# Kernel tuning notes

Measured on AMD Instinct MI355X. Metric: run time of the kernel, lower is better.

Reference implementation:

```python
import jax, jax.numpy as jnp
import numpy as np

E = 128    # embedding_size
N = 8192   # total vertices (64 graphs x 128)
CN = 512   # total color slots
G = 64     # number of graphs
TMAX = 32


def _mlp3(x, W, b):
    # 3-layer MLP: Linear-ReLU-Linear-ReLU-Linear. W: [3,E,E], b: [3,E]
    h = jax.nn.relu(x @ W[0].T + b[0])
    h = jax.nn.relu(h @ W[1].T + b[1])
    return h @ W[2].T + b[2]


def _lstm_cell(x, h, c, Wih, Whh, bih, bhh):
    # PyTorch LSTM gate order: i, f, g, o
    gates = x @ Wih.T + h @ Whh.T + (bih + bhh)
    i, f, g, o = jnp.split(gates, 4, axis=-1)
    c2 = jax.nn.sigmoid(f) * c + jax.nn.sigmoid(i) * jnp.tanh(g)
    h2 = jax.nn.sigmoid(o) * jnp.tanh(c2)
    return h2, c2


def setup_inputs() -> dict:
    key = jax.random.key(0)
    ks = jax.random.split(key, 24)
    s = 1.0 / np.sqrt(E)
    f32 = jnp.float32
    inp = {
        "M_vv": jax.random.normal(ks[0], (N, N), f32) * s,
        "M_vc": jax.random.uniform(ks[1], (N, CN), f32) * (1.0 / np.sqrt(CN)),
        "C": jax.random.normal(ks[2], (CN, E), f32),
        "slice_idx": jnp.full((G,), N // G, dtype=jnp.int32),
        "v_emb_w": jax.random.normal(ks[3], (E, 1), f32) * s,
        "v_emb_b": jax.random.normal(ks[4], (E,), f32) * s,
        "mlpC_W": jax.random.normal(ks[5], (3, E, E), f32) * s,
        "mlpC_b": jax.random.normal(ks[6], (3, E), f32) * s,
        "mlpV_W": jax.random.normal(ks[7], (3, E, E), f32) * s,
        "mlpV_b": jax.random.normal(ks[8], (3, E), f32) * s,
        "Wih_v": jax.random.normal(ks[9], (4 * E, 2 * E), f32) * s,
        "Whh_v": jax.random.normal(ks[10], (4 * E, E), f32) * s,
        "bih_v": jax.random.normal(ks[11], (4 * E,), f32) * s,
        "bhh_v": jax.random.normal(ks[12], (4 * E,), f32) * s,
        "Wih_c": jax.random.normal(ks[13], (4 * E, E), f32) * s,
        "Whh_c": jax.random.normal(ks[14], (4 * E, E), f32) * s,
        "bih_c": jax.random.normal(ks[15], (4 * E,), f32) * s,
        "bhh_c": jax.random.normal(ks[16], (4 * E,), f32) * s,
        "vote_W1": jax.random.normal(ks[17], (E, E), f32) * s,
        "vote_b1": jax.random.normal(ks[18], (E,), f32) * s,
        "vote_W2": jax.random.normal(ks[19], (E, E), f32) * s,
        "vote_b2": jax.random.normal(ks[20], (E,), f32) * s,
        "vote_W3": jax.random.normal(ks[21], (1, E), f32) * s,
        "vote_b3": jax.random.normal(ks[22], (1,), f32) * s,
    }
    return inp


def reference(M_vv, M_vc, C, slice_idx, v_emb_w, v_emb_b, mlpC_W, mlpC_b,
              mlpV_W, mlpV_b, Wih_v, Whh_v, bih_v, bhh_v, Wih_c, Whh_c,
              bih_c, bhh_c, vote_W1, vote_b1, vote_W2, vote_b2, vote_W3, vote_b3):
    n = M_vv.shape[0]
    g = slice_idx.shape[0]
    # V = v_emb(ones(1)) broadcast to all vertices: [N, E]
    v0 = v_emb_w[:, 0] + v_emb_b
    V = jnp.broadcast_to(v0, (n, E))
    # Original torch loop never reassigns V, so both LSTM inputs are
    # loop-invariant; compute them once (identical math, no recompute).
    x_v = jnp.concatenate([M_vv @ V, M_vc @ _mlp3(C, mlpC_W, mlpC_b)], axis=1)  # [N, 2E]
    x_c = M_vc.T @ _mlp3(V, mlpV_W, mlpV_b)                                      # [CN, E]

    def step(carry, _):
        hv, cv, hc, cc = carry
        hv, cv = _lstm_cell(x_v, hv, cv, Wih_v, Whh_v, bih_v, bhh_v)
        hc, cc = _lstm_cell(x_c, hc, cc, Wih_c, Whh_c, bih_c, bhh_c)
        return (hv, cv, hc, cc), None

    init = (V, jnp.zeros_like(V), C, jnp.zeros_like(C))
    (hv, cv, hc, cc), _ = jax.lax.scan(step, init, None, length=TMAX)

    # vote MLP on final vertex hidden state -> [N, 1]
    h = jax.nn.relu(hv @ vote_W1.T + vote_b1)
    h = jax.nn.relu(h @ vote_W2.T + vote_b2)
    v_vote = (h @ vote_W3.T + vote_b3)[:, 0]  # [N]

    # per-graph mean then sigmoid (torch: split + mean + sigmoid + vstack)
    seg = jnp.repeat(jnp.arange(g), slice_idx, total_repeat_length=n)
    sums = jax.ops.segment_sum(v_vote, seg, num_segments=g)
    ret = jax.nn.sigmoid(sums / slice_idx.astype(sums.dtype))
    return (ret, V[None], C)
```

## Files before the change

kernel.cpp:

```cpp
#include <hip/hip_runtime.h>
#include <hip/hip_bf16.h>
#include <stdint.h>


typedef __bf16 bf16x8 __attribute__((ext_vector_type(8)));
typedef float f32x4 __attribute__((ext_vector_type(4)));

#define EDIM 128
#define NVERT 8192
#define CNUM 512
#define NG 64
#define TSTEPS 32

#define WS_CNT 0u
#define WS_V0 32768u
#define WS_W1 33280u
#define WS_BV 35328u
#define WS_ACC 37376u
#define WS_V0BF 37632u
#define WS_MLPC3T 38912u

__device__ __forceinline__ float bf2f(unsigned short s) {
  return __uint_as_float(((unsigned)s) << 16);
}
__device__ __forceinline__ unsigned short f2bf(float f) {
  unsigned u = __float_as_uint(f);
  u += 0x7fffu + ((u >> 16) & 1u);
  return (unsigned short)(u >> 16);
}
__device__ __forceinline__ float sigm(float x) {
  return __builtin_amdgcn_rcpf(1.f + __expf(-x));
}
__device__ __forceinline__ float tanh_f(float x) {
  return 1.f - 2.f * __builtin_amdgcn_rcpf(1.f + __expf(2.f * x));
}
__device__ __forceinline__ f32x4 mfma16(bf16x8 a, bf16x8 b, f32x4 c) {
  return __builtin_amdgcn_mfma_f32_16x16x32_bf16(a, b, c, 0, 0, 0);
}
__device__ __forceinline__ bf16x8 ld8(const float* p) {
  float4 a = *(const float4*)p;
  float4 b = *(const float4*)(p + 4);
  bf16x8 r;
  r[0] = (__bf16)a.x; r[1] = (__bf16)a.y; r[2] = (__bf16)a.z; r[3] = (__bf16)a.w;
  r[4] = (__bf16)b.x; r[5] = (__bf16)b.y; r[6] = (__bf16)b.z; r[7] = (__bf16)b.w;
  return r;
}

__global__ __launch_bounds__(128) void k_setup(
    const float* __restrict__ C, const float* __restrict__ W,
    const float* __restrict__ B, const float* __restrict__ vw,
    const float* __restrict__ vb, const float* __restrict__ Wih,
    const float* __restrict__ bih, const float* __restrict__ bhh,
    float* __restrict__ ws, float* __restrict__ Cout) {
  __shared__ float xb[2][EDIM];
  const int t = threadIdx.x;

  if (blockIdx.x == CNUM) {
    float* v0 = (float*)((char*)ws + WS_V0);
    float* w1 = (float*)((char*)ws + WS_W1);
    float* bvp = (float*)((char*)ws + WS_BV);
    float* acc = (float*)((char*)ws + WS_ACC);
    unsigned short* v0bf = (unsigned short*)((char*)ws + WS_V0BF);
    unsigned int* cnt = (unsigned int*)((char*)ws + WS_CNT);
    float v = vw[t] + vb[t];
    xb[0][t] = v;
    v0[t] = v;
    v0bf[t] = f2bf(v);
    if (t < NG) acc[t] = 0.f;
    if (t == 0) *cnt = 0u;
    __syncthreads();
#pragma unroll
    for (int gi = 0; gi < 4; gi++) {
      const int col = gi * EDIM + t;
      const float4* wr = (const float4*)(Wih + (size_t)col * 256);
      float s = 0.f;
#pragma unroll
      for (int kc = 0; kc < 32; kc++) {
        float4 q = wr[kc];
        const float* xi = xb[0] + kc * 4;
        s += q.x * xi[0] + q.y * xi[1] + q.z * xi[2] + q.w * xi[3];
      }
      w1[col] = s;
      bvp[col] = bih[col] + bhh[col];
    }
    return;
  }

  unsigned short* out_t = (unsigned short*)((char*)ws + WS_MLPC3T);
  const int c = blockIdx.x, e = t;
  float cval = C[c * EDIM + e];
  xb[0][e] = cval;
  Cout[c * EDIM + e] = cval;
  __syncthreads();
#pragma unroll
  for (int l = 0; l < 3; l++) {
    const float4* wrow = (const float4*)(W + ((size_t)l * EDIM + e) * EDIM);
    const float* xin = xb[l & 1];
    float s = B[l * EDIM + e];
#pragma unroll
    for (int kc = 0; kc < EDIM / 4; kc++) {
      float4 q = wrow[kc];
      const float* xi = xin + kc * 4;
      s += q.x * xi[0] + q.y * xi[1] + q.z * xi[2] + q.w * xi[3];
    }
    if (l < 2) {
      s = fmaxf(s, 0.f);
      __syncthreads();
      xb[(l + 1) & 1][e] = s;
      __syncthreads();
    } else {
      out_t[(size_t)e * CNUM + c] = f2bf(s);
    }
  }
}

__global__ __launch_bounds__(512, 1) void k_main(
    const float* __restrict__ Mvv, const float* __restrict__ Mvc,
    const float* __restrict__ Wih, const float* __restrict__ Whh,
    const float* __restrict__ W1, const float* __restrict__ b1,
    const float* __restrict__ W2, const float* __restrict__ b2,
    const float* __restrict__ W3, const float* __restrict__ b3,
    const int* __restrict__ slice, float* __restrict__ ws,
    float* __restrict__ out) {
  const int r0 = blockIdx.x * 32;
  const int t = threadIdx.x;
  const int w = t >> 6;
  const int lane = t & 63;
  const int quad = lane >> 4;
  const int l15 = lane & 15;
  const int nc0 = w * 16;

  __shared__ unsigned short Avc[32][CNUM + 8];
  __shared__ unsigned short Tt[32][EDIM + 8];
  __shared__ unsigned short hv2[2][32][EDIM + 8];
  __shared__ float votes[32];
  __shared__ float rs_s[32];
  __shared__ unsigned int last_s;

  const float* w1v = (const float*)((const char*)ws + WS_W1);
  const float* bvv = (const float*)((const char*)ws + WS_BV);
  float* accg = (float*)((char*)ws + WS_ACC);
  unsigned int* cnt = (unsigned int*)((char*)ws + WS_CNT);
  const unsigned short* v0bf = (const unsigned short*)((const char*)ws + WS_V0BF);
  const unsigned short* m3t = (const unsigned short*)((const char*)ws + WS_MLPC3T);

  {
    const int row = t >> 4, c0 = t & 15;
    const float4* g = (const float4*)(Mvc + (size_t)(r0 + row) * CNUM);
    float4 av[8];
#pragma unroll
    for (int it = 0; it < 8; it++) av[it] = g[it * 16 + c0];

    const float4* mp = (const float4*)(Mvv + (size_t)(r0 + row) * NVERT) + c0;
    float s = 0.f;
#pragma unroll 1
    for (int ch = 0; ch < 8; ch++) {
      float4 q[16];
#pragma unroll
      for (int j = 0; j < 16; j++) q[j] = mp[ch * 256 + j * 16];
#pragma unroll
      for (int j = 0; j < 16; j++) s += q[j].x + q[j].y + q[j].z + q[j].w;
    }
    s += __shfl_down(s, 8, 16);
    s += __shfl_down(s, 4, 16);
    s += __shfl_down(s, 2, 16);
    s += __shfl_down(s, 1, 16);
    if (c0 == 0) rs_s[row] = s;

#pragma unroll
    for (int it = 0; it < 8; it++) {
      int c4 = it * 16 + c0;
      ushort4 h;
      h.x = f2bf(av[it].x); h.y = f2bf(av[it].y);
      h.z = f2bf(av[it].z); h.w = f2bf(av[it].w);
      *(ushort4*)&Avc[row][c4 * 4] = h;
    }
  }
  {
    const float4* v04 = (const float4*)((const char*)ws + WS_V0);
    float4* V4 = (float4*)(out + NG);
#pragma unroll
    for (int i = 0; i < 2; i++) {
      int idx = t + i * 512;
      int vr = idx >> 5, vc = idx & 31;
      V4[(size_t)(r0 + vr) * 32 + vc] = v04[vc];
    }
  }
  for (int i = t; i < 32 * EDIM; i += 512) hv2[0][i >> 7][i & 127] = v0bf[i & 127];
  __syncthreads();

  {
    f32x4 acc[2];
#pragma unroll
    for (int mt = 0; mt < 2; mt++) {
      acc[mt][0] = 0.f; acc[mt][1] = 0.f; acc[mt][2] = 0.f; acc[mt][3] = 0.f;
    }
#pragma unroll
    for (int kc = 0; kc < 16; kc++) {
      bf16x8 a0 = *(const bf16x8*)&Avc[l15][kc * 32 + quad * 8];
      bf16x8 a1 = *(const bf16x8*)&Avc[16 + l15][kc * 32 + quad * 8];
      bf16x8 b0 = *(const bf16x8*)&m3t[(size_t)(nc0 + l15) * CNUM + kc * 32 + quad * 8];
      acc[0] = mfma16(a0, b0, acc[0]);
      acc[1] = mfma16(a1, b0, acc[1]);
    }
#pragma unroll
    for (int mt = 0; mt < 2; mt++)
#pragma unroll
      for (int r = 0; r < 4; r++)
        Tt[mt * 16 + quad * 4 + r][nc0 + l15] = f2bf(acc[mt][r]);
  }
  __syncthreads();

  f32x4 xg[2][4];
  {
    float rsv[2][4];
#pragma unroll
    for (int mt = 0; mt < 2; mt++)
#pragma unroll
      for (int r = 0; r < 4; r++) rsv[mt][r] = rs_s[mt * 16 + quad * 4 + r];
#pragma unroll
    for (int gi = 0; gi < 4; gi++) {
      const int col = gi * 128 + nc0 + l15;
      const float w1c = w1v[col], bvc = bvv[col];
#pragma unroll
      for (int mt = 0; mt < 2; mt++)
#pragma unroll
        for (int r = 0; r < 4; r++) xg[mt][gi][r] = fmaf(rsv[mt][r], w1c, bvc);
    }
#pragma unroll
    for (int kc = 0; kc < 4; kc++) {
      bf16x8 a0 = *(const bf16x8*)&Tt[l15][kc * 32 + quad * 8];
      bf16x8 a1 = *(const bf16x8*)&Tt[16 + l15][kc * 32 + quad * 8];
#pragma unroll
      for (int gi = 0; gi < 4; gi++) {
        const int gcol = gi * 128 + nc0 + l15;
        bf16x8 bfr = ld8(&Wih[(size_t)gcol * 256 + 128 + kc * 32 + quad * 8]);
        xg[0][gi] = mfma16(a0, bfr, xg[0][gi]);
        xg[1][gi] = mfma16(a1, bfr, xg[1][gi]);
      }
    }
  }

  bf16x8 Bh[4][4];
#pragma unroll
  for (int gi = 0; gi < 4; gi++) {
    const int gcol = gi * 128 + nc0 + l15;
#pragma unroll
    for (int kc = 0; kc < 4; kc++)
      Bh[gi][kc] = ld8(&Whh[(size_t)gcol * EDIM + kc * 32 + quad * 8]);
  }

  f32x4 cv[2];
#pragma unroll
  for (int mt = 0; mt < 2; mt++) {
    cv[mt][0] = 0.f; cv[mt][1] = 0.f; cv[mt][2] = 0.f; cv[mt][3] = 0.f;
  }

  int p = 0;
#pragma unroll 1
  for (int step = 0; step < TSTEPS; step++) {
    bf16x8 A[2][4];
#pragma unroll
    for (int mt = 0; mt < 2; mt++)
#pragma unroll
      for (int kc = 0; kc < 4; kc++)
        A[mt][kc] = *(const bf16x8*)&hv2[p][mt * 16 + l15][kc * 32 + quad * 8];
#pragma unroll
    for (int mt = 0; mt < 2; mt++) {
      f32x4 gI = xg[mt][0], gF = xg[mt][1], gG = xg[mt][2], gO = xg[mt][3];
#pragma unroll
      for (int kc = 0; kc < 4; kc++) {
        gI = mfma16(A[mt][kc], Bh[0][kc], gI);
        gF = mfma16(A[mt][kc], Bh[1][kc], gF);
        gG = mfma16(A[mt][kc], Bh[2][kc], gG);
        gO = mfma16(A[mt][kc], Bh[3][kc], gO);
      }
#pragma unroll
      for (int r = 0; r < 4; r++) {
        float ig = sigm(gI[r]), fg = sigm(gF[r]);
        float gg = tanh_f(gG[r]), og = sigm(gO[r]);
        float c2 = fmaf(fg, cv[mt][r], ig * gg);
        cv[mt][r] = c2;
        hv2[p ^ 1][mt * 16 + quad * 4 + r][nc0 + l15] = f2bf(og * tanh_f(c2));
      }
    }
    p ^= 1;
    __syncthreads();
  }

  for (int layer = 0; layer < 2; layer++) {
    const float* Wg = layer ? W2 : W1;
    const float* bg = layer ? b2 : b1;
    bf16x8 A[2][4];
#pragma unroll
    for (int mt = 0; mt < 2; mt++)
#pragma unroll
      for (int kc = 0; kc < 4; kc++)
        A[mt][kc] = *(const bf16x8*)&hv2[0][mt * 16 + l15][kc * 32 + quad * 8];
    f32x4 acc[2];
    {
      float bb = bg[nc0 + l15];
#pragma unroll
      for (int mt = 0; mt < 2; mt++) {
        acc[mt][0] = bb; acc[mt][1] = bb; acc[mt][2] = bb; acc[mt][3] = bb;
      }
    }
#pragma unroll
    for (int kc = 0; kc < 4; kc++) {
      bf16x8 bfr = ld8(&Wg[(size_t)(nc0 + l15) * EDIM + kc * 32 + quad * 8]);
      acc[0] = mfma16(A[0][kc], bfr, acc[0]);
      acc[1] = mfma16(A[1][kc], bfr, acc[1]);
    }
    __syncthreads();
#pragma unroll
    for (int mt = 0; mt < 2; mt++)
#pragma unroll
      for (int r = 0; r < 4; r++)
        hv2[0][mt * 16 + quad * 4 + r][nc0 + l15] = f2bf(fmaxf(acc[mt][r], 0.f));
    __syncthreads();
  }

  {
    const int row = t >> 4, seg = t & 15;
    float part = 0.f;
#pragma unroll
    for (int j = 0; j < 8; j++) {
      const int k = seg * 8 + j;
      part += bf2f(hv2[0][row][k]) * W3[k];
    }
    part += __shfl_down(part, 8, 16);
    part += __shfl_down(part, 4, 16);
    part += __shfl_down(part, 2, 16);
    part += __shfl_down(part, 1, 16);
    if (seg == 0) votes[row] = part + b3[0];
    __syncthreads();
    if (t < 64) {
      float v = (t < 32) ? votes[t] : 0.f;
#pragma unroll
      for (int off = 32; off > 0; off >>= 1) v += __shfl_down(v, off, 64);
      if (t == 0) atomicAdd(&accg[blockIdx.x >> 2], v);
    }
  }

  if (t == 0) {
    __threadfence();
    last_s = atomicAdd(cnt, 1u);
  }
  __syncthreads();
  if (last_s == 4 * NG - 1) {
    __threadfence();
    if (t < NG) {
      float v = __hip_atomic_load(&accg[t], __ATOMIC_ACQUIRE,
                                  __HIP_MEMORY_SCOPE_AGENT);
      float m = v / (float)slice[t];
      out[t] = 1.f / (1.f + __expf(-m));
    }
  }
}

extern "C" void kernel_launch(void* const* d_in, const int* in_sizes, int n_in,
                              void* d_out, int out_size, void* d_ws, size_t ws_size,
                              hipStream_t stream) {
  const float* M_vv = (const float*)d_in[0];
  const float* M_vc = (const float*)d_in[1];
  const float* C = (const float*)d_in[2];
  const int* slice = (const int*)d_in[3];
  const float* vw = (const float*)d_in[4];
  const float* vb = (const float*)d_in[5];
  const float* mW = (const float*)d_in[6];
  const float* mB = (const float*)d_in[7];
  const float* Wih = (const float*)d_in[10];
  const float* Whh = (const float*)d_in[11];
  const float* bih = (const float*)d_in[12];
  const float* bhh = (const float*)d_in[13];
  const float* W1 = (const float*)d_in[18];
  const float* b1 = (const float*)d_in[19];
  const float* W2 = (const float*)d_in[20];
  const float* b2 = (const float*)d_in[21];
  const float* W3 = (const float*)d_in[22];
  const float* b3 = (const float*)d_in[23];
  float* ws = (float*)d_ws;
  float* out = (float*)d_out;

  k_setup<<<CNUM + 1, 128, 0, stream>>>(C, mW, mB, vw, vb, Wih, bih, bhh, ws,
                                        out + NG + (size_t)NVERT * EDIM);
  k_main<<<256, 512, 0, stream>>>(M_vv, M_vc, Wih, Whh, W1, b1, W2, b2, W3, b3,
                                  slice, ws, out);
}
```

Measured before the change: 508.8 us.

## Halve rows per block to launch more blocks across CUs

Each block now handles 16 vertex rows instead of 32, so the grid doubles from 256 to 512 blocks. The launch bound is relaxed to allow several blocks per CU. The intent is to fill all CUs on the device and hide the latency of the serial 32-step LSTM recurrence and the large M_vv row-sum stream. In exchange, each block issues half as many MFMAs per load of the Whh/Wih fragments, so weight reads and per-block setup are duplicated more often, and register pressure under the new bound may cause spills.

```diff
diff --git a/kernel.cpp b/kernel.cpp
--- a/kernel.cpp
+++ b/kernel.cpp
@@ -11,6 +11,7 @@
 #define CNUM 512
 #define NG 64
 #define TSTEPS 32
+#define ROWS 16
 
 #define WS_CNT 0u
 #define WS_V0 32768u
@@ -114,7 +115,7 @@
   }
 }
 
-__global__ __launch_bounds__(512, 1) void k_main(
+__global__ __launch_bounds__(512, 4) void k_main(
     const float* __restrict__ Mvv, const float* __restrict__ Mvc,
     const float* __restrict__ Wih, const float* __restrict__ Whh,
     const float* __restrict__ W1, const float* __restrict__ b1,
@@ -122,7 +123,7 @@
     const float* __restrict__ W3, const float* __restrict__ b3,
     const int* __restrict__ slice, float* __restrict__ ws,
     float* __restrict__ out) {
-  const int r0 = blockIdx.x * 32;
+  const int r0 = blockIdx.x * ROWS;
   const int t = threadIdx.x;
   const int w = t >> 6;
   const int lane = t & 63;
@@ -130,11 +131,11 @@
   const int l15 = lane & 15;
   const int nc0 = w * 16;
 
-  __shared__ unsigned short Avc[32][CNUM + 8];
-  __shared__ unsigned short Tt[32][EDIM + 8];
-  __shared__ unsigned short hv2[2][32][EDIM + 8];
-  __shared__ float votes[32];
-  __shared__ float rs_s[32];
+  __shared__ unsigned short Avc[ROWS][CNUM + 8];
+  __shared__ unsigned short Tt[ROWS][EDIM + 8];
+  __shared__ unsigned short hv2[2][ROWS][EDIM + 8];
+  __shared__ float votes[ROWS];
+  __shared__ float rs_s[ROWS];
   __shared__ unsigned int last_s;
 
   const float* w1v = (const float*)((const char*)ws + WS_W1);
@@ -145,31 +146,32 @@
   const unsigned short* m3t = (const unsigned short*)((const char*)ws + WS_MLPC3T);
 
   {
-    const int row = t >> 4, c0 = t & 15;
+    const int row = t >> 5, c0 = t & 31;
     const float4* g = (const float4*)(Mvc + (size_t)(r0 + row) * CNUM);
-    float4 av[8];
-#pragma unroll
-    for (int it = 0; it < 8; it++) av[it] = g[it * 16 + c0];
+    float4 av[4];
+#pragma unroll
+    for (int it = 0; it < 4; it++) av[it] = g[it * 32 + c0];
 
     const float4* mp = (const float4*)(Mvv + (size_t)(r0 + row) * NVERT) + c0;
     float s = 0.f;
 #pragma unroll 1
-    for (int ch = 0; ch < 8; ch++) {
+    for (int ch = 0; ch < 4; ch++) {
       float4 q[16];
 #pragma unroll
-      for (int j = 0; j < 16; j++) q[j] = mp[ch * 256 + j * 16];
+      for (int j = 0; j < 16; j++) q[j] = mp[ch * 512 + j * 32];
 #pragma unroll
       for (int j = 0; j < 16; j++) s += q[j].x + q[j].y + q[j].z + q[j].w;
     }
-    s += __shfl_down(s, 8, 16);
-    s += __shfl_down(s, 4, 16);
-    s += __shfl_down(s, 2, 16);
-    s += __shfl_down(s, 1, 16);
+    s += __shfl_down(s, 16, 32);
+    s += __shfl_down(s, 8, 32);
+    s += __shfl_down(s, 4, 32);
+    s += __shfl_down(s, 2, 32);
+    s += __shfl_down(s, 1, 32);
     if (c0 == 0) rs_s[row] = s;
 
 #pragma unroll
-    for (int it = 0; it < 8; it++) {
-      int c4 = it * 16 + c0;
+    for (int it = 0; it < 4; it++) {
+      int c4 = it * 32 + c0;
       ushort4 h;
       h.x = f2bf(av[it].x); h.y = f2bf(av[it].y);
       h.z = f2bf(av[it].z); h.w = f2bf(av[it].w);
@@ -179,64 +181,47 @@
   {
     const float4* v04 = (const float4*)((const char*)ws + WS_V0);
     float4* V4 = (float4*)(out + NG);
-#pragma unroll
-    for (int i = 0; i < 2; i++) {
-      int idx = t + i * 512;
-      int vr = idx >> 5, vc = idx & 31;
-      V4[(size_t)(r0 + vr) * 32 + vc] = v04[vc];
-    }
-  }
-  for (int i = t; i < 32 * EDIM; i += 512) hv2[0][i >> 7][i & 127] = v0bf[i & 127];
+    int vr = t >> 5, vc = t & 31;
+    V4[(size_t)(r0 + vr) * 32 + vc] = v04[vc];
+  }
+  for (int i = t; i < ROWS * EDIM; i += 512) hv2[0][i >> 7][i & 127] = v0bf[i & 127];
   __syncthreads();
 
   {
-    f32x4 acc[2];
-#pragma unroll
-    for (int mt = 0; mt < 2; mt++) {
-      acc[mt][0] = 0.f; acc[mt][1] = 0.f; acc[mt][2] = 0.f; acc[mt][3] = 0.f;
-    }
+    f32x4 acc;
+    acc[0] = 0.f; acc[1] = 0.f; acc[2] = 0.f; acc[3] = 0.f;
 #pragma unroll
     for (int kc = 0; kc < 16; kc++) {
       bf16x8 a0 = *(const bf16x8*)&Avc[l15][kc * 32 + quad * 8];
-      bf16x8 a1 = *(const bf16x8*)&Avc[16 + l15][kc * 32 + quad * 8];
       bf16x8 b0 = *(const bf16x8*)&m3t[(size_t)(nc0 + l15) * CNUM + kc * 32 + quad * 8];
-      acc[0] = mfma16(a0, b0, acc[0]);
-      acc[1] = mfma16(a1, b0, acc[1]);
-    }
-#pragma unroll
-    for (int mt = 0; mt < 2; mt++)
-#pragma unroll
-      for (int r = 0; r < 4; r++)
-        Tt[mt * 16 + quad * 4 + r][nc0 + l15] = f2bf(acc[mt][r]);
+      acc = mfma16(a0, b0, acc);
+    }
+#pragma unroll
+    for (int r = 0; r < 4; r++)
+      Tt[quad * 4 + r][nc0 + l15] = f2bf(acc[r]);
   }
   __syncthreads();
 
-  f32x4 xg[2][4];
-  {
-    float rsv[2][4];
-#pragma unroll
-    for (int mt = 0; mt < 2; mt++)
-#pragma unroll
-      for (int r = 0; r < 4; r++) rsv[mt][r] = rs_s[mt * 16 + quad * 4 + r];
+  f32x4 xg[4];
+  {
+    float rsv[4];
+#pragma unroll
+    for (int r = 0; r < 4; r++) rsv[r] = rs_s[quad * 4 + r];
 #pragma unroll
     for (int gi = 0; gi < 4; gi++) {
       const int col = gi * 128 + nc0 + l15;
       const float w1c = w1v[col], bvc = bvv[col];
 #pragma unroll
-      for (int mt = 0; mt < 2; mt++)
-#pragma unroll
-        for (int r = 0; r < 4; r++) xg[mt][gi][r] = fmaf(rsv[mt][r], w1c, bvc);
+      for (int r = 0; r < 4; r++) xg[gi][r] = fmaf(rsv[r], w1c, bvc);
     }
 #pragma unroll
     for (int kc = 0; kc < 4; kc++) {
       bf16x8 a0 = *(const bf16x8*)&Tt[l15][kc * 32 + quad * 8];
-      bf16x8 a1 = *(const bf16x8*)&Tt[16 + l15][kc * 32 + quad * 8];
 #pragma unroll
       for (int gi = 0; gi < 4; gi++) {
         const int gcol = gi * 128 + nc0 + l15;
         bf16x8 bfr = ld8(&Wih[(size_t)gcol * 256 + 128 + kc * 32 + quad * 8]);
-        xg[0][gi] = mfma16(a0, bfr, xg[0][gi]);
-        xg[1][gi] = mfma16(a1, bfr, xg[1][gi]);
+        xg[gi] = mfma16(a0, bfr, xg[gi]);
       }
     }
   }
@@ -250,39 +235,31 @@
       Bh[gi][kc] = ld8(&Whh[(size_t)gcol * EDIM + kc * 32 + quad * 8]);
   }
 
-  f32x4 cv[2];
-#pragma unroll
-  for (int mt = 0; mt < 2; mt++) {
-    cv[mt][0] = 0.f; cv[mt][1] = 0.f; cv[mt][2] = 0.f; cv[mt][3] = 0.f;
-  }
+  f32x4 cv;
+  cv[0] = 0.f; cv[1] = 0.f; cv[2] = 0.f; cv[3] = 0.f;
 
   int p = 0;
 #pragma unroll 1
   for (int step = 0; step < TSTEPS; step++) {
-    bf16x8 A[2][4];
-#pragma unroll
-    for (int mt = 0; mt < 2; mt++)
-#pragma unroll
-      for (int kc = 0; kc < 4; kc++)
-        A[mt][kc] = *(const bf16x8*)&hv2[p][mt * 16 + l15][kc * 32 + quad * 8];
-#pragma unroll
-    for (int mt = 0; mt < 2; mt++) {
-      f32x4 gI = xg[mt][0], gF = xg[mt][1], gG = xg[mt][2], gO = xg[mt][3];
-#pragma unroll
-      for (int kc = 0; kc < 4; kc++) {
-        gI = mfma16(A[mt][kc], Bh[0][kc], gI);
-        gF = mfma16(A[mt][kc], Bh[1][kc], gF);
-        gG = mfma16(A[mt][kc], Bh[2][kc], gG);
-        gO = mfma16(A[mt][kc], Bh[3][kc], gO);
-      }
-#pragma unroll
-      for (int r = 0; r < 4; r++) {
-        float ig = sigm(gI[r]), fg = sigm(gF[r]);
-        float gg = tanh_f(gG[r]), og = sigm(gO[r]);
-        float c2 = fmaf(fg, cv[mt][r], ig * gg);
-        cv[mt][r] = c2;
-        hv2[p ^ 1][mt * 16 + quad * 4 + r][nc0 + l15] = f2bf(og * tanh_f(c2));
-      }
+    bf16x8 A[4];
+#pragma unroll
+    for (int kc = 0; kc < 4; kc++)
+      A[kc] = *(const bf16x8*)&hv2[p][l15][kc * 32 + quad * 8];
+    f32x4 gI = xg[0], gF = xg[1], gG = xg[2], gO = xg[3];
+#pragma unroll
+    for (int kc = 0; kc < 4; kc++) {
+      gI = mfma16(A[kc], Bh[0][kc], gI);
+      gF = mfma16(A[kc], Bh[1][kc], gF);
+      gG = mfma16(A[kc], Bh[2][kc], gG);
+      gO = mfma16(A[kc], Bh[3][kc], gO);
+    }
+#pragma unroll
+    for (int r = 0; r < 4; r++) {
+      float ig = sigm(gI[r]), fg = sigm(gF[r]);
+      float gg = tanh_f(gG[r]), og = sigm(gO[r]);
+      float c2 = fmaf(fg, cv[r], ig * gg);
+      cv[r] = c2;
+      hv2[p ^ 1][quad * 4 + r][nc0 + l15] = f2bf(og * tanh_f(c2));
     }
     p ^= 1;
     __syncthreads();
@@ -291,54 +268,48 @@
   for (int layer = 0; layer < 2; layer++) {
     const float* Wg = layer ? W2 : W1;
     const float* bg = layer ? b2 : b1;
-    bf16x8 A[2][4];
-#pragma unroll
-    for (int mt = 0; mt < 2; mt++)
-#pragma unroll
-      for (int kc = 0; kc < 4; kc++)
-        A[mt][kc] = *(const bf16x8*)&hv2[0][mt * 16 + l15][kc * 32 + quad * 8];
-    f32x4 acc[2];
+    bf16x8 A[4];
+#pragma unroll
+    for (int kc = 0; kc < 4; kc++)
+      A[kc] = *(const bf16x8*)&hv2[0][l15][kc * 32 + quad * 8];
+    f32x4 acc;
     {
       float bb = bg[nc0 + l15];
-#pragma unroll
-      for (int mt = 0; mt < 2; mt++) {
-        acc[mt][0] = bb; acc[mt][1] = bb; acc[mt][2] = bb; acc[mt][3] = bb;
-      }
+      acc[0] = bb; acc[1] = bb; acc[2] = bb; acc[3] = bb;
     }
 #pragma unroll
     for (int kc = 0; kc < 4; kc++) {
       bf16x8 bfr = ld8(&Wg[(size_t)(nc0 + l15) * EDIM + kc * 32 + quad * 8]);
-      acc[0] = mfma16(A[0][kc], bfr, acc[0]);
-      acc[1] = mfma16(A[1][kc], bfr, acc[1]);
-    }
-    __syncthreads();
-#pragma unroll
-    for (int mt = 0; mt < 2; mt++)
-#pragma unroll
-      for (int r = 0; r < 4; r++)
-        hv2[0][mt * 16 + quad * 4 + r][nc0 + l15] = f2bf(fmaxf(acc[mt][r], 0.f));
-    __syncthreads();
-  }
-
-  {
-    const int row = t >> 4, seg = t & 15;
-    float part = 0.f;
-#pragma unroll
-    for (int j = 0; j < 8; j++) {
-      const int k = seg * 8 + j;
-      part += bf2f(hv2[0][row][k]) * W3[k];
-    }
-    part += __shfl_down(part, 8, 16);
-    part += __shfl_down(part, 4, 16);
-    part += __shfl_down(part, 2, 16);
-    part += __shfl_down(part, 1, 16);
-    if (seg == 0) votes[row] = part + b3[0];
+      acc = mfma16(A[kc], bfr, acc);
+    }
+    __syncthreads();
+#pragma unroll
+    for (int r = 0; r < 4; r++)
+      hv2[0][quad * 4 + r][nc0 + l15] = f2bf(fmaxf(acc[r], 0.f));
+    __syncthreads();
+  }
+
+  {
+    if (t < 16 * ROWS) {
+      const int row = t >> 4, seg = t & 15;
+      float part = 0.f;
+#pragma unroll
+      for (int j = 0; j < 8; j++) {
+        const int k = seg * 8 + j;
+        part += bf2f(hv2[0][row][k]) * W3[k];
+      }
+      part += __shfl_down(part, 8, 16);
+      part += __shfl_down(part, 4, 16);
+      part += __shfl_down(part, 2, 16);
+      part += __shfl_down(part, 1, 16);
+      if (seg == 0) votes[row] = part + b3[0];
+    }
     __syncthreads();
     if (t < 64) {
-      float v = (t < 32) ? votes[t] : 0.f;
+      float v = (t < ROWS) ? votes[t] : 0.f;
 #pragma unroll
       for (int off = 32; off > 0; off >>= 1) v += __shfl_down(v, off, 64);
-      if (t == 0) atomicAdd(&accg[blockIdx.x >> 2], v);
+      if (t == 0) atomicAdd(&accg[blockIdx.x >> 3], v);
     }
   }
 
@@ -347,7 +318,7 @@
     last_s = atomicAdd(cnt, 1u);
   }
   __syncthreads();
-  if (last_s == 4 * NG - 1) {
+  if (last_s == 8 * NG - 1) {
     __threadfence();
     if (t < NG) {
       float v = __hip_atomic_load(&accg[t], __ATOMIC_ACQUIRE,
@@ -384,6 +355,6 @@
 
   k_setup<<<CNUM + 1, 128, 0, stream>>>(C, mW, mB, vw, vb, Wih, bih, bhh, ws,
                                         out + NG + (size_t)NVERT * EDIM);
-  k_main<<<256, 512, 0, stream>>>(M_vv, M_vc, Wih, Whh, W1, b1, W2, b2, W3, b3,
-                                  slice, ws, out);
-}
+  k_main<<<NVERT / ROWS, 512, 0, stream>>>(M_vv, M_vc, Wih, Whh, W1, b1, W2,
+                                           b2, W3, b3, slice, ws, out);
+}
```

New measurement: 504.4 us. No clear change (-0.9%).
